# Optimization experiments

Hardware: AMD Instinct MI355X
Metric: run time of the kernel (lower is better)

Reference implementation:

```python
import jax, jax.numpy as jnp
import numpy as np

BATCH = 4096
INDIM = 1024
OUTDIM = 1024
NNZ = 52224  # min(1024,1024) * int(1024 * 0.05)


def setup_inputs() -> dict:
    key = jax.random.key(0)
    k1, k2, k3, k4, k5 = jax.random.split(key, 5)
    stdv = np.sqrt(2.0 / INDIM).astype(np.float32)
    input_ = jax.random.normal(k1, (BATCH, INDIM), dtype=jnp.float32)
    weight = jax.random.normal(k2, (NNZ,), dtype=jnp.float32) * stdv
    bias = jax.random.normal(k3, (OUTDIM,), dtype=jnp.float32) * stdv
    ind_in = jax.random.randint(k4, (NNZ,), 0, INDIM, dtype=jnp.int32)
    ind_out = jax.random.randint(k5, (NNZ,), 0, OUTDIM, dtype=jnp.int32)
    return {"input_": input_, "weight": weight, "bias": bias,
            "ind_in": ind_in, "ind_out": ind_out}


def reference(input_, weight, bias, ind_in, ind_out):
    # x = input_[:, ind_in] * weight        [B, NNZ]
    gathered = input_[:, ind_in] * weight
    # scatter_add into output columns       [B, OUTDIM]
    out = jnp.zeros((input_.shape[0], OUTDIM), dtype=input_.dtype)
    out = out.at[:, ind_out].add(gathered)
    return out + bias
```

## Files before the change

kernel.cpp:

```cpp
#include <hip/hip_runtime.h>
#include <stdint.h>

#define INDIM   1024
#define OUTDIM  1024
#define BM 64
#define BN 64
#define BK 64
#define KTILES (INDIM / BK)

typedef __attribute__((ext_vector_type(8))) short  short8;
typedef __attribute__((ext_vector_type(4))) float  floatx4;

__device__ __forceinline__ uint32_t bf16pack(float x, float y) {
    uint32_t ux = __float_as_uint(x);
    ux = ((ux + 0x7FFFu + ((ux >> 16) & 1u)) >> 16) & 0xFFFFu;
    uint32_t uy = __float_as_uint(y);
    uy = (uy + 0x7FFFu + ((uy >> 16) & 1u)) & 0xFFFF0000u;
    return ux | uy;
}

__device__ __forceinline__ uint32_t bf16lo(float x) {
    uint32_t u = __float_as_uint(x);
    return ((u + 0x7FFFu + ((u >> 16) & 1u)) >> 16) & 0xFFFFu;
}

__device__ __forceinline__ void atomic_pk_add_bf16(uint32_t* addr, uint32_t val) {
    asm volatile("global_atomic_pk_add_bf16 %0, %1, off"
                 :: "v"(addr), "v"(val) : "memory");
}

__global__ __launch_bounds__(256) void k_prep(
    const int* __restrict__ ind_in, const int* __restrict__ ind_out,
    const float* __restrict__ wgt, int nnz,
    const float4* __restrict__ A32, int nA4,
    uint32_t* __restrict__ W16T, uint2* __restrict__ A16)
{
    const int gtid   = blockIdx.x * 256 + threadIdx.x;
    const int stride = gridDim.x * 256;

    if (gtid < nnz) {
        const uint32_t idx = ((uint32_t)ind_out[gtid] << 10) | (uint32_t)ind_in[gtid];
        const uint32_t w16 = bf16lo(wgt[gtid]);
        atomic_pk_add_bf16(W16T + (idx >> 1), (idx & 1) ? (w16 << 16) : w16);
    }

    for (int j = gtid; j < nA4; j += stride) {
        float4 v = A32[j];
        A16[j] = make_uint2(bf16pack(v.x, v.y), bf16pack(v.z, v.w));
    }
}

__device__ __forceinline__ void gload_lds16(const ushort* g, ushort* l) {
    __builtin_amdgcn_global_load_lds(
        (const __attribute__((address_space(1))) void*)g,
        (__attribute__((address_space(3))) void*)l, 16, 0, 0);
}

__global__ __launch_bounds__(256, 4) void k_gemm(
    const ushort* __restrict__ A16,
    const ushort* __restrict__ W16T,
    const float* __restrict__ bias,
    float* __restrict__ C, int M)
{
    __shared__ ushort lA[2][BM * BK];
    __shared__ ushort lB[2][BN * BK];

    const int t      = threadIdx.x;
    const int w      = t >> 6;
    const int L      = t & 63;
    const int lane15 = L & 15;
    const int quad   = L >> 4;
    const int wm     = w >> 1, wn = w & 1;

    const int bid = blockIdx.x;
    const int bm0 = ((bid & 7) * 8 + (bid >> 7)) * BM;
    const int bn0 = ((bid >> 3) & 15) * BN;

    const int srow = t >> 3;
    const int j8   = (t & 7) ^ (srow & 7);

    const ushort* As = A16  + (size_t)(bm0 + srow) * INDIM + j8 * 8;
    const ushort* Bs = W16T + (size_t)(bn0 + srow) * INDIM + j8 * 8;

    const int dbase = w * 512;

    auto STAGE = [&](int buf, int kt) {
        const int g = kt * BK;
        gload_lds16(As + g,              &lA[buf][dbase]);
        gload_lds16(As + g + 32 * INDIM, &lA[buf][dbase + 2048]);
        gload_lds16(Bs + g,              &lB[buf][dbase]);
        gload_lds16(Bs + g + 32 * INDIM, &lB[buf][dbase + 2048]);
    };

    floatx4 acc[2][2] = {};

    auto COMPUTE = [&](int buf) {
        #pragma unroll
        for (int ks = 0; ks < 2; ++ks) {
            const int j = ks * 4 + quad;
            short8 af[2], bf[2];
            #pragma unroll
            for (int tm = 0; tm < 2; ++tm) {
                const int row = wm * 32 + tm * 16 + lane15;
                af[tm] = *(const short8*)(&lA[buf][row * BK + ((j ^ (row & 7)) << 3)]);
            }
            #pragma unroll
            for (int tn = 0; tn < 2; ++tn) {
                const int row = wn * 32 + tn * 16 + lane15;
                bf[tn] = *(const short8*)(&lB[buf][row * BK + ((j ^ (row & 7)) << 3)]);
            }
            #pragma unroll
            for (int tm = 0; tm < 2; ++tm)
                #pragma unroll
                for (int tn = 0; tn < 2; ++tn)
                    acc[tm][tn] = __builtin_amdgcn_mfma_f32_16x16x32_bf16(
                        af[tm], bf[tn], acc[tm][tn], 0, 0, 0);
        }
    };

    STAGE(0, 0);
    #pragma unroll 2
    for (int kt = 0; kt < KTILES - 1; ++kt) {
        STAGE((kt + 1) & 1, kt + 1);
        asm volatile("s_waitcnt vmcnt(4)" ::: "memory");
        __builtin_amdgcn_s_barrier();
        __builtin_amdgcn_sched_barrier(0);
        COMPUTE(kt & 1);
        __builtin_amdgcn_sched_barrier(0);
        __builtin_amdgcn_s_barrier();
    }
    asm volatile("s_waitcnt vmcnt(0)" ::: "memory");
    __builtin_amdgcn_s_barrier();
    __builtin_amdgcn_sched_barrier(0);
    COMPUTE((KTILES - 1) & 1);

    #pragma unroll
    for (int tm = 0; tm < 2; ++tm) {
        #pragma unroll
        for (int tn = 0; tn < 2; ++tn) {
            const int col = bn0 + wn * 32 + tn * 16 + lane15;
            const float bv = bias[col];
            #pragma unroll
            for (int r = 0; r < 4; ++r) {
                const int row = bm0 + wm * 32 + tm * 16 + quad * 4 + r;
                __builtin_nontemporal_store(acc[tm][tn][r] + bv,
                                            &C[(size_t)row * OUTDIM + col]);
            }
        }
    }
}

extern "C" void kernel_launch(void* const* d_in, const int* in_sizes, int n_in,
                              void* d_out, int out_size, void* d_ws, size_t ws_size,
                              hipStream_t stream) {
    const float* input  = (const float*)d_in[0];
    const float* weight = (const float*)d_in[1];
    const float* bias   = (const float*)d_in[2];
    const int*   ind_in  = (const int*)d_in[3];
    const int*   ind_out = (const int*)d_in[4];
    float* out = (float*)d_out;

    const int nnz = in_sizes[1];
    const int M   = out_size / OUTDIM;
    const int nA4 = M * INDIM / 4;

    char* ws = (char*)d_ws;
    ushort* W16T = (ushort*)ws;
    ushort* A16  = (ushort*)(ws + (2u << 20));

    k_prep<<<2048, 256, 0, stream>>>(ind_in, ind_out, weight, nnz,
                                     (const float4*)input, nA4,
                                     (uint32_t*)W16T, (uint2*)A16);
    k_gemm<<<(M / BM) * (OUTDIM / BN), 256, 0, stream>>>(A16, W16T, bias, out, M);
}
```

Baseline: 92.65 us.

## Fuse fp32-to-bf16 input conversion into GEMM tile loading

Removes the separate conversion pass that wrote a bf16 copy of the input. The GEMM now loads fp32 A tiles into registers, converts them to bf16 and writes them to LDS, pipelined around the MFMA compute. The prep kernel is reduced to the weight scatter only. This saves a full read and write of the activation matrix. In exchange the GEMM reads twice the A bytes per tile, adds conversion ALU work, and moves A from async global-to-LDS loads to register staging.

```diff
diff --git a/kernel.cpp b/kernel.cpp
--- a/kernel.cpp
+++ b/kernel.cpp
@@ -29,24 +29,15 @@
                  :: "v"(addr), "v"(val) : "memory");
 }
 
-__global__ __launch_bounds__(256) void k_prep(
+__global__ __launch_bounds__(256) void k_scatter(
     const int* __restrict__ ind_in, const int* __restrict__ ind_out,
-    const float* __restrict__ wgt, int nnz,
-    const float4* __restrict__ A32, int nA4,
-    uint32_t* __restrict__ W16T, uint2* __restrict__ A16)
+    const float* __restrict__ wgt, int nnz, uint32_t* __restrict__ W16T)
 {
-    const int gtid   = blockIdx.x * 256 + threadIdx.x;
-    const int stride = gridDim.x * 256;
-
-    if (gtid < nnz) {
-        const uint32_t idx = ((uint32_t)ind_out[gtid] << 10) | (uint32_t)ind_in[gtid];
-        const uint32_t w16 = bf16lo(wgt[gtid]);
+    const int g = blockIdx.x * 256 + threadIdx.x;
+    if (g < nnz) {
+        const uint32_t idx = ((uint32_t)ind_out[g] << 10) | (uint32_t)ind_in[g];
+        const uint32_t w16 = bf16lo(wgt[g]);
         atomic_pk_add_bf16(W16T + (idx >> 1), (idx & 1) ? (w16 << 16) : w16);
-    }
-
-    for (int j = gtid; j < nA4; j += stride) {
-        float4 v = A32[j];
-        A16[j] = make_uint2(bf16pack(v.x, v.y), bf16pack(v.z, v.w));
     }
 }
 
@@ -57,7 +48,7 @@
 }
 
 __global__ __launch_bounds__(256, 4) void k_gemm(
-    const ushort* __restrict__ A16,
+    const float* __restrict__ A32,
     const ushort* __restrict__ W16T,
     const float* __restrict__ bias,
     float* __restrict__ C, int M)
@@ -79,17 +70,34 @@
     const int srow = t >> 3;
     const int j8   = (t & 7) ^ (srow & 7);
 
-    const ushort* As = A16  + (size_t)(bm0 + srow) * INDIM + j8 * 8;
     const ushort* Bs = W16T + (size_t)(bn0 + srow) * INDIM + j8 * 8;
+    const float*  Aa = A32  + (size_t)(bm0 + srow) * INDIM + j8 * 8;
 
     const int dbase = w * 512;
+    const int wAoff = srow * 64 + (t & 7) * 8;
 
-    auto STAGE = [&](int buf, int kt) {
+    auto STAGE_W = [&](int buf, int kt) {
         const int g = kt * BK;
-        gload_lds16(As + g,              &lA[buf][dbase]);
-        gload_lds16(As + g + 32 * INDIM, &lA[buf][dbase + 2048]);
         gload_lds16(Bs + g,              &lB[buf][dbase]);
         gload_lds16(Bs + g + 32 * INDIM, &lB[buf][dbase + 2048]);
+    };
+
+    float4 ar[4];
+    auto A_LOAD = [&](int kt) {
+        const float* p = Aa + kt * BK;
+        ar[0] = *(const float4*)(p);
+        ar[1] = *(const float4*)(p + 4);
+        ar[2] = *(const float4*)(p + (size_t)32 * INDIM);
+        ar[3] = *(const float4*)(p + (size_t)32 * INDIM + 4);
+    };
+    auto CVT_WRITE = [&](int buf) {
+        uint4 v0, v1;
+        v0.x = bf16pack(ar[0].x, ar[0].y); v0.y = bf16pack(ar[0].z, ar[0].w);
+        v0.z = bf16pack(ar[1].x, ar[1].y); v0.w = bf16pack(ar[1].z, ar[1].w);
+        v1.x = bf16pack(ar[2].x, ar[2].y); v1.y = bf16pack(ar[2].z, ar[2].w);
+        v1.z = bf16pack(ar[3].x, ar[3].y); v1.w = bf16pack(ar[3].z, ar[3].w);
+        *(uint4*)(&lA[buf][wAoff])        = v0;
+        *(uint4*)(&lA[buf][wAoff + 2048]) = v1;
     };
 
     floatx4 acc[2][2] = {};
@@ -118,14 +126,26 @@
         }
     };
 
-    STAGE(0, 0);
-    #pragma unroll 2
+    A_LOAD(0);
+    STAGE_W(0, 0);
+    __builtin_amdgcn_sched_barrier(0);
+    asm volatile("s_waitcnt vmcnt(2)" ::: "memory");
+    CVT_WRITE(0);
+    asm volatile("s_waitcnt lgkmcnt(0)" ::: "memory");
+    __builtin_amdgcn_sched_barrier(0);
+
     for (int kt = 0; kt < KTILES - 1; ++kt) {
-        STAGE((kt + 1) & 1, kt + 1);
-        asm volatile("s_waitcnt vmcnt(4)" ::: "memory");
+        A_LOAD(kt + 1);
+        STAGE_W((kt + 1) & 1, kt + 1);
+        __builtin_amdgcn_sched_barrier(0);
+        asm volatile("s_waitcnt vmcnt(6)" ::: "memory");
         __builtin_amdgcn_s_barrier();
         __builtin_amdgcn_sched_barrier(0);
         COMPUTE(kt & 1);
+        __builtin_amdgcn_sched_barrier(0);
+        asm volatile("s_waitcnt vmcnt(2)" ::: "memory");
+        CVT_WRITE((kt + 1) & 1);
+        asm volatile("s_waitcnt lgkmcnt(0)" ::: "memory");
         __builtin_amdgcn_sched_barrier(0);
         __builtin_amdgcn_s_barrier();
     }
@@ -162,14 +182,11 @@
 
     const int nnz = in_sizes[1];
     const int M   = out_size / OUTDIM;
-    const int nA4 = M * INDIM / 4;
 
     char* ws = (char*)d_ws;
     ushort* W16T = (ushort*)ws;
-    ushort* A16  = (ushort*)(ws + (2u << 20));
 
-    k_prep<<<2048, 256, 0, stream>>>(ind_in, ind_out, weight, nnz,
-                                     (const float4*)input, nA4,
-                                     (uint32_t*)W16T, (uint2*)A16);
-    k_gemm<<<(M / BM) * (OUTDIM / BN), 256, 0, stream>>>(A16, W16T, bias, out, M);
+    k_scatter<<<(nnz + 255) / 256, 256, 0, stream>>>(ind_in, ind_out, weight,
+                                                     nnz, (uint32_t*)W16T);
+    k_gemm<<<(M / BM) * (OUTDIM / BN), 256, 0, stream>>>(input, W16T, bias, out, M);
 }
```

After: 104.6 us. 12.9% more time.
